# Performance work log

Hardware: AMD Instinct MI355X
Metric: run time of the kernel (lower is better)

The kernel has to match this reference:

```python
import jax, jax.numpy as jnp
import numpy as np

B, S, HID = 2, 2048, 1024
H, HKV, D = 16, 8, 128
G = H // HKV  # GQA group size
EPS = 1e-6
THETA = 1000000.0


def setup_inputs() -> dict:
    key = jax.random.key(0)
    ks = jax.random.split(key, 6)
    hidden_states = jax.random.normal(ks[0], (B, S, HID), dtype=jnp.float32)
    # causal boolean mask: True = attend
    attention_mask = jnp.tril(jnp.ones((S, S), dtype=bool))[None, None]
    # RoPE tables (HF convention: freqs duplicated across both halves)
    inv_freq = 1.0 / (THETA ** (jnp.arange(0, D, 2, dtype=jnp.float32) / D))
    ang = jnp.arange(S, dtype=jnp.float32)[:, None] * inv_freq[None, :]  # [S, D/2]
    emb = jnp.concatenate([ang, ang], axis=-1)  # [S, D]
    cos, sin = jnp.cos(emb), jnp.sin(emb)
    std = 0.02
    Wq = jax.random.normal(ks[1], (HID, H * D), dtype=jnp.float32) * std
    Wk = jax.random.normal(ks[2], (HID, HKV * D), dtype=jnp.float32) * std
    Wv = jax.random.normal(ks[3], (HID, HKV * D), dtype=jnp.float32) * std
    Wo = jax.random.normal(ks[4], (H * D, HID), dtype=jnp.float32) * std
    q_norm_w = jnp.ones((D,), dtype=jnp.float32)
    k_norm_w = jnp.ones((D,), dtype=jnp.float32)
    return {"hidden_states": hidden_states, "attention_mask": attention_mask,
            "cos": cos, "sin": sin, "Wq": Wq, "Wk": Wk, "Wv": Wv, "Wo": Wo,
            "q_norm_w": q_norm_w, "k_norm_w": k_norm_w}


def _rms_norm(x, w):
    var = jnp.mean(x * x, axis=-1, keepdims=True)
    return x * jax.lax.rsqrt(var + EPS) * w


def _rotate_half(x):
    x1, x2 = jnp.split(x, 2, axis=-1)
    return jnp.concatenate([-x2, x1], axis=-1)


def reference(hidden_states, attention_mask, cos, sin, Wq, Wk, Wv, Wo, q_norm_w, k_norm_w):
    b, s, _ = hidden_states.shape
    xq = (hidden_states @ Wq).reshape(b, s, H, D).transpose(0, 2, 1, 3)    # [B,H,S,D]
    xk = (hidden_states @ Wk).reshape(b, s, HKV, D).transpose(0, 2, 1, 3)  # [B,Hkv,S,D]
    xv = (hidden_states @ Wv).reshape(b, s, HKV, D).transpose(0, 2, 1, 3)  # [B,Hkv,S,D]
    xq = _rms_norm(xq, q_norm_w)
    xk = _rms_norm(xk, k_norm_w)
    c = cos[None, None]  # [1,1,S,D]
    si = sin[None, None]
    xq = xq * c + _rotate_half(xq) * si
    xk = xk * c + _rotate_half(xk) * si
    # GQA without materializing repeated KV: group q heads per kv head
    xqg = xq.reshape(b, HKV, G, s, D)
    scale = 1.0 / jnp.sqrt(jnp.asarray(D, dtype=xq.dtype))
    scores = jnp.einsum('bkgsd,bktd->bkgst', xqg, xk) * scale  # [B,Hkv,G,S,S]
    mask = attention_mask[:, :, None]  # [1,1,1,S,S]
    scores = jnp.where(mask, scores, jnp.asarray(-jnp.inf, dtype=scores.dtype))
    probs = jax.nn.softmax(scores, axis=-1)
    out = jnp.einsum('bkgst,bktd->bkgsd', probs, xv)  # [B,Hkv,G,S,D]
    out = out.reshape(b, H, s, D).transpose(0, 2, 1, 3).reshape(b, s, H * D)
    return out @ Wo
```

## Files before the change

kernel.cpp:

```cpp
#include <hip/hip_runtime.h>
#include <stdint.h>

#define B_ 2
#define S_ 2048
#define H_ 16
#define HKV_ 8
#define D_ 128
#define EPS_ 1e-6f
#define SCALE_ 0.08838834764831845f
#define QSZ_ 8388608
#define KSZ_ 4194304

typedef __attribute__((ext_vector_type(8))) __bf16 bf16x8;
typedef __attribute__((ext_vector_type(4))) float f32x4;
typedef __attribute__((ext_vector_type(16))) float f32x16;

static __device__ __forceinline__ uint16_t f2b(float f) {
  uint32_t u = __builtin_bit_cast(uint32_t, f);
  u += 0x7fffu + ((u >> 16) & 1u);
  return (uint16_t)(u >> 16);
}
static __device__ __forceinline__ float b2f(uint16_t b) {
  uint32_t u = ((uint32_t)b) << 16;
  return __builtin_bit_cast(float, u);
}

typedef const __attribute__((address_space(1))) uint32_t* gas_p;
typedef __attribute__((address_space(3))) uint32_t* las_p;
static __device__ __forceinline__ void gload16(const void* g, void* l) {
  __builtin_amdgcn_global_load_lds((gas_p)g, (las_p)l, 16, 0, 0);
}

__global__ void castk(const float* __restrict__ in, uint16_t* __restrict__ out) {
  int i = blockIdx.x * 256 + threadIdx.x;
  float4 f = ((const float4*)in)[i];
  uint2 o;
  o.x = (uint32_t)f2b(f.x) | ((uint32_t)f2b(f.y) << 16);
  o.y = (uint32_t)f2b(f.z) | ((uint32_t)f2b(f.w) << 16);
  ((uint2*)out)[i] = o;
}

__global__ void transcast(const float* __restrict__ Wm, uint16_t* __restrict__ Wt,
                          int K, int N) {
  __shared__ float t[32][33];
  int nb = blockIdx.x * 32, kb = blockIdx.y * 32;
  int tx = threadIdx.x & 31, ty = threadIdx.x >> 5;
  #pragma unroll
  for (int i = ty; i < 32; i += 8) t[i][tx] = Wm[(size_t)(kb + i) * N + nb + tx];
  __syncthreads();
  #pragma unroll
  for (int i = ty; i < 32; i += 8) Wt[(size_t)(nb + i) * K + kb + tx] = f2b(t[tx][i]);
}

__global__ __launch_bounds__(256) void vtrans(const uint16_t* __restrict__ Vin,
                                              uint16_t* __restrict__ Vt) {
  __shared__ uint16_t L[64 * 64];
  int s0 = blockIdx.x * 64, d0 = blockIdx.y * 64;
  const uint16_t* src = Vin + (size_t)blockIdx.z * S_ * D_;
  uint16_t* dst = Vt + (size_t)blockIdx.z * S_ * D_;
  int t = threadIdx.x;
  int rr = t >> 3, cb = t & 7;
  #pragma unroll
  for (int half = 0; half < 2; ++half) {
    int row = rr + half * 32;
    uint4 v = *(const uint4*)(src + (size_t)(s0 + row) * D_ + d0 + cb * 8);
    *(uint4*)(L + row * 64 + ((cb ^ (row & 7)) * 8)) = v;
  }
  __syncthreads();
  int dr = t >> 2, sc = (t & 3) * 16;
  union { uint16_t s[16]; uint4 q[2]; } u;
  #pragma unroll
  for (int j = 0; j < 16; ++j) {
    int s = sc + j;
    u.s[j] = L[s * 64 + (((dr >> 3) ^ (s & 7)) * 8) + (dr & 7)];
  }
  uint4* op = (uint4*)(dst + (size_t)(d0 + dr) * S_ + s0 + sc);
  op[0] = u.q[0];
  op[1] = u.q[1];
}

__global__ __launch_bounds__(256) void gemm_bt(const uint16_t* __restrict__ A,
                                               const uint16_t* __restrict__ Bt,
                                               void* __restrict__ Cout,
                                               int M, int N, int K, int mode) {
  __shared__ uint16_t Al[128 * 64];
  __shared__ uint16_t Bl[128 * 64];
  int tid = threadIdx.x;
  int lane = tid & 63, lr = lane & 15, g = lane >> 4;
  int w = tid >> 6, wm = w >> 1, wn = w & 1;
  int wbase = w * 64;
  int m0 = blockIdx.y * 128, n0 = blockIdx.x * 128;
  f32x4 acc[4][4] = {};
  for (int k0 = 0; k0 < K; k0 += 64) {
    __syncthreads();
    #pragma unroll
    for (int p = 0; p < 4; ++p) {
      int c = tid + p * 256;
      int row = c >> 3, cb = c & 7;
      int sc = (cb ^ (row & 7)) * 8;
      gload16(A + (size_t)(m0 + row) * K + k0 + sc, Al + (size_t)(p * 256 + wbase) * 8);
      gload16(Bt + (size_t)(n0 + row) * K + k0 + sc, Bl + (size_t)(p * 256 + wbase) * 8);
    }
    __syncthreads();
    #pragma unroll
    for (int ks = 0; ks < 2; ++ks) {
      bf16x8 af[4], bfr[4];
      #pragma unroll
      for (int mi = 0; mi < 4; ++mi) {
        int row = wm * 64 + mi * 16 + lr;
        af[mi] = *(bf16x8*)((char*)Al + row * 128 + ((ks * 64 + g * 16) ^ ((row & 7) << 4)));
      }
      #pragma unroll
      for (int ni = 0; ni < 4; ++ni) {
        int row = wn * 64 + ni * 16 + lr;
        bfr[ni] = *(bf16x8*)((char*)Bl + row * 128 + ((ks * 64 + g * 16) ^ ((row & 7) << 4)));
      }
      __builtin_amdgcn_s_setprio(1);
      #pragma unroll
      for (int mi = 0; mi < 4; ++mi)
        #pragma unroll
        for (int ni = 0; ni < 4; ++ni)
          acc[mi][ni] = __builtin_amdgcn_mfma_f32_16x16x32_bf16(af[mi], bfr[ni], acc[mi][ni], 0, 0, 0);
      __builtin_amdgcn_s_setprio(0);
    }
  }
  #pragma unroll
  for (int mi = 0; mi < 4; ++mi)
    #pragma unroll
    for (int ni = 0; ni < 4; ++ni)
      #pragma unroll
      for (int e = 0; e < 4; ++e) {
        int row = m0 + wm * 64 + mi * 16 + 4 * g + e;
        int col = n0 + wn * 64 + ni * 16 + lr;
        float v = acc[mi][ni][e];
        if (mode == 2) {
          ((float*)Cout)[(size_t)row * N + col] = v;
        } else {
          int bb = row >> 11, s = row & 2047;
          size_t off;
          if (col < 2048)
            off = (((size_t)(bb * 16 + (col >> 7))) * 2048 + s) * 128 + (col & 127);
          else if (col < 3072)
            off = QSZ_ + (((size_t)(bb * 8 + ((col - 2048) >> 7))) * 2048 + s) * 128 + (col & 127);
          else
            off = QSZ_ + KSZ_ + (((size_t)(bb * 8 + ((col - 3072) >> 7))) * 2048 + s) * 128 + (col & 127);
          ((uint16_t*)Cout)[off] = f2b(v);
        }
      }
}

__global__ __launch_bounds__(256) void gemm_o(const uint16_t* __restrict__ A,
                                              const uint16_t* __restrict__ Bt,
                                              float* __restrict__ Cout,
                                              int M, int N, int K) {
  __shared__ uint16_t Al[128 * 64];
  __shared__ uint16_t Bl[64 * 64];
  int tid = threadIdx.x;
  int lane = tid & 63, lr = lane & 15, g = lane >> 4;
  int w = tid >> 6, wm = w >> 1, wn = w & 1;
  int wbase = w * 64;
  int m0 = blockIdx.y * 128, n0 = blockIdx.x * 64;
  f32x4 acc[4][2] = {};
  for (int k0 = 0; k0 < K; k0 += 64) {
    __syncthreads();
    #pragma unroll
    for (int p = 0; p < 4; ++p) {
      int c = tid + p * 256;
      int row = c >> 3, cb = c & 7;
      int sc = (cb ^ (row & 7)) * 8;
      gload16(A + (size_t)(m0 + row) * K + k0 + sc, Al + (size_t)(p * 256 + wbase) * 8);
    }
    #pragma unroll
    for (int p = 0; p < 2; ++p) {
      int c = tid + p * 256;
      int row = c >> 3, cb = c & 7;
      int sc = (cb ^ (row & 7)) * 8;
      gload16(Bt + (size_t)(n0 + row) * K + k0 + sc, Bl + (size_t)(p * 256 + wbase) * 8);
    }
    __syncthreads();
    #pragma unroll
    for (int ks = 0; ks < 2; ++ks) {
      bf16x8 af[4], bfr[2];
      #pragma unroll
      for (int mi = 0; mi < 4; ++mi) {
        int row = wm * 64 + mi * 16 + lr;
        af[mi] = *(bf16x8*)((char*)Al + row * 128 + ((ks * 64 + g * 16) ^ ((row & 7) << 4)));
      }
      #pragma unroll
      for (int ni = 0; ni < 2; ++ni) {
        int row = wn * 32 + ni * 16 + lr;
        bfr[ni] = *(bf16x8*)((char*)Bl + row * 128 + ((ks * 64 + g * 16) ^ ((row & 7) << 4)));
      }
      __builtin_amdgcn_s_setprio(1);
      #pragma unroll
      for (int mi = 0; mi < 4; ++mi)
        #pragma unroll
        for (int ni = 0; ni < 2; ++ni)
          acc[mi][ni] = __builtin_amdgcn_mfma_f32_16x16x32_bf16(af[mi], bfr[ni], acc[mi][ni], 0, 0, 0);
      __builtin_amdgcn_s_setprio(0);
    }
  }
  #pragma unroll
  for (int mi = 0; mi < 4; ++mi)
    #pragma unroll
    for (int ni = 0; ni < 2; ++ni)
      #pragma unroll
      for (int e = 0; e < 4; ++e) {
        int row = m0 + wm * 64 + mi * 16 + 4 * g + e;
        int col = n0 + wn * 32 + ni * 16 + lr;
        Cout[(size_t)row * N + col] = acc[mi][ni][e];
      }
}

__global__ void norm_rope(uint16_t* __restrict__ Qb, uint16_t* __restrict__ Kb,
                          const float* __restrict__ qw, const float* __restrict__ kw,
                          const float* __restrict__ cosr, const float* __restrict__ sinr) {
  int row = blockIdx.x * 4 + (threadIdx.x >> 6);
  int lane = threadIdx.x & 63;
  int hh = row % 24;
  int bs = row / 24;
  int b = bs >> 11, s = bs & 2047;
  uint16_t* ptr;
  const float* wv;
  float sc;
  if (hh < H_) { ptr = Qb + (((size_t)(b * H_ + hh)) * S_ + s) * D_; wv = qw; sc = SCALE_; }
  else         { ptr = Kb + (((size_t)(b * HKV_ + (hh - H_))) * S_ + s) * D_; wv = kw; sc = 1.0f; }
  float x1 = b2f(ptr[lane]), x2 = b2f(ptr[lane + 64]);
  float ss = x1 * x1 + x2 * x2;
  #pragma unroll
  for (int msk = 1; msk < 64; msk <<= 1) ss += __shfl_xor(ss, msk, 64);
  float r = rsqrtf(ss * (1.0f / 128.0f) + EPS_);
  float n1 = x1 * r * wv[lane], n2 = x2 * r * wv[lane + 64];
  float c1 = cosr[s * 128 + lane], s1 = sinr[s * 128 + lane];
  float c2 = cosr[s * 128 + lane + 64], s2 = sinr[s * 128 + lane + 64];
  ptr[lane]      = f2b((n1 * c1 - n2 * s1) * sc);
  ptr[lane + 64] = f2b((n2 * c2 + n1 * s2) * sc);
}

#define STAGE(BUF, KB) {                                                       \
  int kb64 = (KB) * 64;                                                        \
  _Pragma("unroll") for (int p2 = 0; p2 < 4; ++p2) {                           \
    int ck = p2 * 4 + w;                                                       \
    int krow = ck * 4 + (lane >> 4);                                           \
    int kg = (lane & 15) ^ (krow & 7);                                         \
    gload16(Kg + (size_t)(kb64 + krow) * D_ + kg * 8, Kl[BUF] + ck * 512);     \
    int vrow = ck * 8 + (lane >> 3);                                           \
    int vg = (lane & 7) ^ (vrow & 7);                                          \
    gload16(Vg + (size_t)vrow * S_ + kb64 + vg * 8, Vl[BUF] + ck * 512);       \
  } }

__global__ __launch_bounds__(256, 2) void attn_kernel(const uint16_t* __restrict__ Qb,
                                                      const uint16_t* __restrict__ Kb,
                                                      const uint16_t* __restrict__ Vtg,
                                                      uint16_t* __restrict__ out) {
  __shared__ uint16_t Kl[2][64 * 128];
  __shared__ uint16_t Vl[2][128 * 64];
  int tid = threadIdx.x, lane = tid & 63, w = tid >> 6;
  int ql = lane & 31, hi = lane >> 5;
  int bi = blockIdx.x;
  int biH = bi >> 8;
  int j = bi & 255;
  int qgl = j >> 5;
  int qg = biH ? qgl : 15 - qgl;
  int rem = j & 31;
  int bkv = rem >> 1, hsel = rem & 1;
  int b = bkv >> 3, kv = bkv & 7, h = kv * 2 + hsel;
  int qt = qg * 4 + w;
  int q0 = qt * 32;
  int mykb = qt >> 1;
  int kbmax = 2 * qg + 1;
  const uint16_t* Qg = Qb + ((size_t)(b * H_ + h)) * S_ * D_;
  const uint16_t* Kg = Kb + ((size_t)(b * HKV_ + kv)) * S_ * D_;
  const uint16_t* Vg = Vtg + ((size_t)(b * HKV_ + kv)) * S_ * D_;
  bf16x8 qf[8];
  #pragma unroll
  for (int t = 0; t < 8; ++t)
    qf[t] = *(const bf16x8*)(Qg + (size_t)(q0 + ql) * D_ + t * 16 + 8 * hi);
  f32x16 O[4] = {};
  float mrun = -__builtin_inff();
  float lrun = 0.f;
  STAGE(0, 0)
  for (int kb = 0; kb <= kbmax; ++kb) {
    int cur = kb & 1;
    __syncthreads();
    if (kb < kbmax) STAGE(cur ^ 1, kb + 1)
    if (kb <= mykb) {
      const uint16_t* KlC = Kl[cur];
      const uint16_t* VlC = Vl[cur];
      bool diag = (kb == mykb);
      bool skip2 = diag && ((qt & 1) == 0);
      float p0[16], p1[16];
      {
        bf16x8 kf[8];
        #pragma unroll
        for (int t = 0; t < 8; ++t)
          kf[t] = *(const bf16x8*)(KlC + ql * 128 + (((2 * t + hi) ^ (ql & 7)) * 8));
        f32x16 acc = {};
        __builtin_amdgcn_s_setprio(1);
        #pragma unroll
        for (int t = 0; t < 8; ++t)
          acc = __builtin_amdgcn_mfma_f32_32x32x16_bf16(kf[t], qf[t], acc, 0, 0, 0);
        __builtin_amdgcn_s_setprio(0);
        #pragma unroll
        for (int r = 0; r < 16; ++r) p0[r] = acc[r];
      }
      if (!skip2) {
        bf16x8 kf[8];
        #pragma unroll
        for (int t = 0; t < 8; ++t)
          kf[t] = *(const bf16x8*)(KlC + (32 + ql) * 128 + (((2 * t + hi) ^ (ql & 7)) * 8));
        f32x16 acc = {};
        __builtin_amdgcn_s_setprio(1);
        #pragma unroll
        for (int t = 0; t < 8; ++t)
          acc = __builtin_amdgcn_mfma_f32_32x32x16_bf16(kf[t], qf[t], acc, 0, 0, 0);
        __builtin_amdgcn_s_setprio(0);
        #pragma unroll
        for (int r = 0; r < 16; ++r) p1[r] = acc[r];
      }
      if (diag && !(qt & 1)) {
        #pragma unroll
        for (int r = 0; r < 16; ++r) {
          int kk = kb * 64 + 8 * (r >> 2) + 4 * hi + (r & 3);
          if (kk > q0 + ql) p0[r] = -__builtin_inff();
        }
      }
      if (diag && (qt & 1)) {
        #pragma unroll
        for (int r = 0; r < 16; ++r) {
          int kk = kb * 64 + 32 + 8 * (r >> 2) + 4 * hi + (r & 3);
          if (kk > q0 + ql) p1[r] = -__builtin_inff();
        }
      }
      float m8[8];
      #pragma unroll
      for (int i = 0; i < 8; ++i) m8[i] = fmaxf(p0[i], p0[i + 8]);
      if (!skip2) {
        #pragma unroll
        for (int i = 0; i < 8; ++i) m8[i] = fmaxf(m8[i], fmaxf(p1[i], p1[i + 8]));
      }
      float m4a = fmaxf(m8[0], m8[4]), m4b = fmaxf(m8[1], m8[5]);
      float m4c = fmaxf(m8[2], m8[6]), m4d = fmaxf(m8[3], m8[7]);
      float pmax = fmaxf(fmaxf(m4a, m4b), fmaxf(m4c, m4d));
      pmax = fmaxf(pmax, __shfl_xor(pmax, 32, 64));
      if (__any(pmax > mrun + 8.f)) {
        float mnew = fmaxf(mrun, pmax);
        float rs = __expf(mrun - mnew);
        lrun *= rs;
        #pragma unroll
        for (int r = 0; r < 16; ++r) {
          float rr = __shfl(rs, (r & 3) + 8 * (r >> 2) + 4 * hi, 64);
          #pragma unroll
          for (int dt = 0; dt < 4; ++dt) O[dt][r] *= rr;
        }
        mrun = mnew;
      }
      float ls = 0.f;
      union PW { uint32_t w[4]; bf16x8 v; } pa0, pa1;
      #pragma unroll
      for (int r = 0; r < 16; ++r) { p0[r] = __expf(p0[r] - mrun); ls += p0[r]; }
      {
        uint32_t uu[4][2];
        #pragma unroll
        for (int T = 0; T < 4; ++T) {
          asm("v_cvt_pk_bf16_f32 %0, %1, %2" : "=v"(uu[T][0]) : "v"(p0[4 * T]), "v"(p0[4 * T + 1]));
          asm("v_cvt_pk_bf16_f32 %0, %1, %2" : "=v"(uu[T][1]) : "v"(p0[4 * T + 2]), "v"(p0[4 * T + 3]));
        }
        uint32_t a = uu[0][0], bb2 = uu[1][0];
        asm("v_permlane32_swap_b32 %0, %1" : "+v"(a), "+v"(bb2));
        uint32_t c = uu[0][1], d = uu[1][1];
        asm("v_permlane32_swap_b32 %0, %1" : "+v"(c), "+v"(d));
        pa0.w[0] = a; pa0.w[1] = c; pa0.w[2] = bb2; pa0.w[3] = d;
        uint32_t a2 = uu[2][0], b2 = uu[3][0];
        asm("v_permlane32_swap_b32 %0, %1" : "+v"(a2), "+v"(b2));
        uint32_t c2 = uu[2][1], d2 = uu[3][1];
        asm("v_permlane32_swap_b32 %0, %1" : "+v"(c2), "+v"(d2));
        pa1.w[0] = a2; pa1.w[1] = c2; pa1.w[2] = b2; pa1.w[3] = d2;
      }
      __builtin_amdgcn_s_setprio(1);
      #pragma unroll
      for (int dt = 0; dt < 4; ++dt) {
        bf16x8 v0 = *(const bf16x8*)(VlC + (dt * 32 + ql) * 64 + (((0 + hi) ^ (ql & 7)) * 8));
        bf16x8 v1 = *(const bf16x8*)(VlC + (dt * 32 + ql) * 64 + (((2 + hi) ^ (ql & 7)) * 8));
        O[dt] = __builtin_amdgcn_mfma_f32_32x32x16_bf16(pa0.v, v0, O[dt], 0, 0, 0);
        O[dt] = __builtin_amdgcn_mfma_f32_32x32x16_bf16(pa1.v, v1, O[dt], 0, 0, 0);
      }
      __builtin_amdgcn_s_setprio(0);
      if (!skip2) {
        union PW pa2, pa3;
        #pragma unroll
        for (int r = 0; r < 16; ++r) { p1[r] = __expf(p1[r] - mrun); ls += p1[r]; }
        {
          uint32_t uu[4][2];
          #pragma unroll
          for (int T = 0; T < 4; ++T) {
            asm("v_cvt_pk_bf16_f32 %0, %1, %2" : "=v"(uu[T][0]) : "v"(p1[4 * T]), "v"(p1[4 * T + 1]));
            asm("v_cvt_pk_bf16_f32 %0, %1, %2" : "=v"(uu[T][1]) : "v"(p1[4 * T + 2]), "v"(p1[4 * T + 3]));
          }
          uint32_t a = uu[0][0], bb2 = uu[1][0];
          asm("v_permlane32_swap_b32 %0, %1" : "+v"(a), "+v"(bb2));
          uint32_t c = uu[0][1], d = uu[1][1];
          asm("v_permlane32_swap_b32 %0, %1" : "+v"(c), "+v"(d));
          pa2.w[0] = a; pa2.w[1] = c; pa2.w[2] = bb2; pa2.w[3] = d;
          uint32_t a2 = uu[2][0], b2 = uu[3][0];
          asm("v_permlane32_swap_b32 %0, %1" : "+v"(a2), "+v"(b2));
          uint32_t c2 = uu[2][1], d2 = uu[3][1];
          asm("v_permlane32_swap_b32 %0, %1" : "+v"(c2), "+v"(d2));
          pa3.w[0] = a2; pa3.w[1] = c2; pa3.w[2] = b2; pa3.w[3] = d2;
        }
        __builtin_amdgcn_s_setprio(1);
        #pragma unroll
        for (int dt = 0; dt < 4; ++dt) {
          bf16x8 v2 = *(const bf16x8*)(VlC + (dt * 32 + ql) * 64 + (((4 + hi) ^ (ql & 7)) * 8));
          bf16x8 v3 = *(const bf16x8*)(VlC + (dt * 32 + ql) * 64 + (((6 + hi) ^ (ql & 7)) * 8));
          O[dt] = __builtin_amdgcn_mfma_f32_32x32x16_bf16(pa2.v, v2, O[dt], 0, 0, 0);
          O[dt] = __builtin_amdgcn_mfma_f32_32x32x16_bf16(pa3.v, v3, O[dt], 0, 0, 0);
        }
        __builtin_amdgcn_s_setprio(0);
      }
      ls += __shfl_xor(ls, 32, 64);
      lrun += ls;
    }
  }
  float linv = 1.0f / lrun;
  #pragma unroll
  for (int r = 0; r < 16; ++r) {
    int qrl = (r & 3) + 8 * (r >> 2) + 4 * hi;
    float lr_ = __shfl(linv, qrl, 64);
    #pragma unroll
    for (int dt = 0; dt < 4; ++dt) {
      size_t o = ((size_t)(b * S_ + q0 + qrl)) * 2048 + h * 128 + dt * 32 + ql;
      out[o] = f2b(O[dt][r] * lr_);
    }
  }
}

extern "C" void kernel_launch(void* const* d_in, const int* in_sizes, int n_in,
                              void* d_out, int out_size, void* d_ws, size_t ws_size,
                              hipStream_t stream) {
  const float* hidden = (const float*)d_in[0];
  const float* cosr = (const float*)d_in[2];
  const float* sinr = (const float*)d_in[3];
  const float* Wq = (const float*)d_in[4];
  const float* Wk = (const float*)d_in[5];
  const float* Wv = (const float*)d_in[6];
  const float* Wo = (const float*)d_in[7];
  const float* qw = (const float*)d_in[8];
  const float* kw = (const float*)d_in[9];

  uint16_t* p = (uint16_t*)d_ws;
  uint16_t* Xb   = p; p += (size_t)4096 * 1024;
  uint16_t* Wqt  = p; p += (size_t)2048 * 1024;
  uint16_t* Wkt  = p; p += (size_t)1024 * 1024;
  uint16_t* Wvt  = p; p += (size_t)1024 * 1024;
  uint16_t* Wot  = p; p += (size_t)1024 * 2048;
  uint16_t* Qbuf = p; p += (size_t)B_ * H_ * S_ * D_;
  uint16_t* Kbuf = p; p += (size_t)B_ * HKV_ * S_ * D_;
  uint16_t* Vbuf = p; p += (size_t)B_ * HKV_ * S_ * D_;
  uint16_t* attn = p; p += (size_t)4096 * 2048;
  uint16_t* Vtb  = Xb;

  castk<<<4096, 256, 0, stream>>>(hidden, Xb);
  transcast<<<dim3(64, 32), 256, 0, stream>>>(Wq, Wqt, 1024, 2048);
  transcast<<<dim3(32, 32), 256, 0, stream>>>(Wk, Wkt, 1024, 1024);
  transcast<<<dim3(32, 32), 256, 0, stream>>>(Wv, Wvt, 1024, 1024);
  transcast<<<dim3(32, 64), 256, 0, stream>>>(Wo, Wot, 2048, 1024);
  gemm_bt<<<dim3(32, 32), 256, 0, stream>>>(Xb, Wqt, Qbuf, 4096, 4096, 1024, 3);
  vtrans<<<dim3(32, 2, 16), 256, 0, stream>>>(Vbuf, Vtb);
  norm_rope<<<24576, 256, 0, stream>>>(Qbuf, Kbuf, qw, kw, cosr, sinr);
  attn_kernel<<<512, 256, 0, stream>>>(Qbuf, Kbuf, Vtb, attn);
  gemm_o<<<dim3(16, 32), 256, 0, stream>>>(attn, Wot, (float*)d_out, 4096, 1024, 2048);
}
```

Baseline: 194.5 us.

## Fuse RMSNorm, RoPE and V transpose into QKV GEMM epilogue; merge prep kernels

The cast and four weight-transpose kernels are merged into one prep launch. The QKV GEMM now stages its output tile in LDS, and its epilogue applies RMSNorm, RoPE and Q scaling for Q/K tiles and writes V already transposed. This removes the separate norm_rope and vtrans kernels, their global round trips and several launches. In exchange the GEMM epilogue uses many registers (64 floats per thread) and issues strided scalar loads of the weight and cos/sin tables.

```diff
diff --git a/kernel.cpp b/kernel.cpp
--- a/kernel.cpp
+++ b/kernel.cpp
@@ -8,8 +8,6 @@
 #define D_ 128
 #define EPS_ 1e-6f
 #define SCALE_ 0.08838834764831845f
-#define QSZ_ 8388608
-#define KSZ_ 4194304
 
 typedef __attribute__((ext_vector_type(8))) __bf16 bf16x8;
 typedef __attribute__((ext_vector_type(4))) float f32x4;
@@ -31,75 +29,69 @@
   __builtin_amdgcn_global_load_lds((gas_p)g, (las_p)l, 16, 0, 0);
 }
 
-__global__ void castk(const float* __restrict__ in, uint16_t* __restrict__ out) {
-  int i = blockIdx.x * 256 + threadIdx.x;
-  float4 f = ((const float4*)in)[i];
-  uint2 o;
-  o.x = (uint32_t)f2b(f.x) | ((uint32_t)f2b(f.y) << 16);
-  o.y = (uint32_t)f2b(f.z) | ((uint32_t)f2b(f.w) << 16);
-  ((uint2*)out)[i] = o;
-}
-
-__global__ void transcast(const float* __restrict__ Wm, uint16_t* __restrict__ Wt,
-                          int K, int N) {
-  __shared__ float t[32][33];
-  int nb = blockIdx.x * 32, kb = blockIdx.y * 32;
+__global__ __launch_bounds__(256) void prep(const float* __restrict__ hidden,
+                                            uint16_t* __restrict__ Xb,
+                                            const float* __restrict__ Wq,
+                                            const float* __restrict__ Wk,
+                                            const float* __restrict__ Wv,
+                                            const float* __restrict__ Wo,
+                                            uint16_t* __restrict__ Wqt,
+                                            uint16_t* __restrict__ Wkt,
+                                            uint16_t* __restrict__ Wvt,
+                                            uint16_t* __restrict__ Wot) {
+  __shared__ float tt[32][33];
+  int bid = blockIdx.x;
+  if (bid < 4096) {
+    int i = bid * 256 + threadIdx.x;
+    float4 f = ((const float4*)hidden)[i];
+    uint2 o;
+    o.x = (uint32_t)f2b(f.x) | ((uint32_t)f2b(f.y) << 16);
+    o.y = (uint32_t)f2b(f.z) | ((uint32_t)f2b(f.w) << 16);
+    ((uint2*)Xb)[i] = o;
+    return;
+  }
+  bid -= 4096;
+  const float* src; uint16_t* dst; int K, N, bx, by;
+  if (bid < 2048)       { src = Wq; dst = Wqt; K = 1024; N = 2048; bx = bid & 63; by = bid >> 6; }
+  else if (bid < 3072)  { bid -= 2048; src = Wk; dst = Wkt; K = 1024; N = 1024; bx = bid & 31; by = bid >> 5; }
+  else if (bid < 4096)  { bid -= 3072; src = Wv; dst = Wvt; K = 1024; N = 1024; bx = bid & 31; by = bid >> 5; }
+  else                  { bid -= 4096; src = Wo; dst = Wot; K = 2048; N = 1024; bx = bid & 31; by = bid >> 5; }
+  int nb = bx * 32, kb = by * 32;
   int tx = threadIdx.x & 31, ty = threadIdx.x >> 5;
   #pragma unroll
-  for (int i = ty; i < 32; i += 8) t[i][tx] = Wm[(size_t)(kb + i) * N + nb + tx];
+  for (int i = ty; i < 32; i += 8) tt[i][tx] = src[(size_t)(kb + i) * N + nb + tx];
   __syncthreads();
   #pragma unroll
-  for (int i = ty; i < 32; i += 8) Wt[(size_t)(nb + i) * K + kb + tx] = f2b(t[tx][i]);
-}
-
-__global__ __launch_bounds__(256) void vtrans(const uint16_t* __restrict__ Vin,
-                                              uint16_t* __restrict__ Vt) {
-  __shared__ uint16_t L[64 * 64];
-  int s0 = blockIdx.x * 64, d0 = blockIdx.y * 64;
-  const uint16_t* src = Vin + (size_t)blockIdx.z * S_ * D_;
-  uint16_t* dst = Vt + (size_t)blockIdx.z * S_ * D_;
-  int t = threadIdx.x;
-  int rr = t >> 3, cb = t & 7;
-  #pragma unroll
-  for (int half = 0; half < 2; ++half) {
-    int row = rr + half * 32;
-    uint4 v = *(const uint4*)(src + (size_t)(s0 + row) * D_ + d0 + cb * 8);
-    *(uint4*)(L + row * 64 + ((cb ^ (row & 7)) * 8)) = v;
-  }
-  __syncthreads();
-  int dr = t >> 2, sc = (t & 3) * 16;
-  union { uint16_t s[16]; uint4 q[2]; } u;
-  #pragma unroll
-  for (int j = 0; j < 16; ++j) {
-    int s = sc + j;
-    u.s[j] = L[s * 64 + (((dr >> 3) ^ (s & 7)) * 8) + (dr & 7)];
-  }
-  uint4* op = (uint4*)(dst + (size_t)(d0 + dr) * S_ + s0 + sc);
-  op[0] = u.q[0];
-  op[1] = u.q[1];
-}
-
-__global__ __launch_bounds__(256) void gemm_bt(const uint16_t* __restrict__ A,
-                                               const uint16_t* __restrict__ Bt,
-                                               void* __restrict__ Cout,
-                                               int M, int N, int K, int mode) {
-  __shared__ uint16_t Al[128 * 64];
-  __shared__ uint16_t Bl[128 * 64];
+  for (int i = ty; i < 32; i += 8) dst[(size_t)(nb + i) * K + kb + tx] = f2b(tt[tx][i]);
+}
+
+__global__ __launch_bounds__(256) void gemm_qkv(const uint16_t* __restrict__ A,
+                                                const uint16_t* __restrict__ Bt,
+                                                uint16_t* __restrict__ Qb,
+                                                uint16_t* __restrict__ Kb,
+                                                uint16_t* __restrict__ Vtb,
+                                                const float* __restrict__ qw,
+                                                const float* __restrict__ kw,
+                                                const float* __restrict__ cosr,
+                                                const float* __restrict__ sinr) {
+  __shared__ uint16_t Sh[128 * 128];
+  uint16_t* Al = Sh;
+  uint16_t* Bl = Sh + 128 * 64;
   int tid = threadIdx.x;
   int lane = tid & 63, lr = lane & 15, g = lane >> 4;
   int w = tid >> 6, wm = w >> 1, wn = w & 1;
   int wbase = w * 64;
   int m0 = blockIdx.y * 128, n0 = blockIdx.x * 128;
   f32x4 acc[4][4] = {};
-  for (int k0 = 0; k0 < K; k0 += 64) {
+  for (int k0 = 0; k0 < 1024; k0 += 64) {
     __syncthreads();
     #pragma unroll
     for (int p = 0; p < 4; ++p) {
       int c = tid + p * 256;
       int row = c >> 3, cb = c & 7;
       int sc = (cb ^ (row & 7)) * 8;
-      gload16(A + (size_t)(m0 + row) * K + k0 + sc, Al + (size_t)(p * 256 + wbase) * 8);
-      gload16(Bt + (size_t)(n0 + row) * K + k0 + sc, Bl + (size_t)(p * 256 + wbase) * 8);
+      gload16(A + (size_t)(m0 + row) * 1024 + k0 + sc, Al + (size_t)(p * 256 + wbase) * 8);
+      gload16(Bt + (size_t)(n0 + row) * 1024 + k0 + sc, Bl + (size_t)(p * 256 + wbase) * 8);
     }
     __syncthreads();
     #pragma unroll
@@ -124,29 +116,75 @@
       __builtin_amdgcn_s_setprio(0);
     }
   }
+  __syncthreads();
+  uint16_t* L = Sh;
   #pragma unroll
   for (int mi = 0; mi < 4; ++mi)
     #pragma unroll
     for (int ni = 0; ni < 4; ++ni)
       #pragma unroll
       for (int e = 0; e < 4; ++e) {
-        int row = m0 + wm * 64 + mi * 16 + 4 * g + e;
-        int col = n0 + wn * 64 + ni * 16 + lr;
-        float v = acc[mi][ni][e];
-        if (mode == 2) {
-          ((float*)Cout)[(size_t)row * N + col] = v;
-        } else {
-          int bb = row >> 11, s = row & 2047;
-          size_t off;
-          if (col < 2048)
-            off = (((size_t)(bb * 16 + (col >> 7))) * 2048 + s) * 128 + (col & 127);
-          else if (col < 3072)
-            off = QSZ_ + (((size_t)(bb * 8 + ((col - 2048) >> 7))) * 2048 + s) * 128 + (col & 127);
-          else
-            off = QSZ_ + KSZ_ + (((size_t)(bb * 8 + ((col - 3072) >> 7))) * 2048 + s) * 128 + (col & 127);
-          ((uint16_t*)Cout)[off] = f2b(v);
-        }
-      }
+        int row = wm * 64 + mi * 16 + 4 * g + e;
+        int col = wn * 64 + ni * 16 + lr;
+        L[row * 128 + ((((col >> 3) ^ (row & 7)) << 3) | (col & 7))] = f2b(acc[mi][ni][e]);
+      }
+  __syncthreads();
+  int hsel = n0 >> 7;
+  if (hsel < 24) {
+    int row = tid >> 1, half = tid & 1;
+    int gr = m0 + row, bb = gr >> 11, s = gr & 2047;
+    int d0 = half * 32;
+    float x[64];
+    #pragma unroll
+    for (int c8 = 0; c8 < 8; ++c8) {
+      int j = (c8 & 3) * 8 + d0 + (c8 >> 2) * 64;
+      union { bf16x8 v; uint16_t u[8]; } tmp;
+      tmp.v = *(bf16x8*)(L + row * 128 + (((j >> 3) ^ (row & 7)) << 3));
+      #pragma unroll
+      for (int k = 0; k < 8; ++k) x[c8 * 8 + k] = b2f(tmp.u[k]);
+    }
+    float ss = 0.f;
+    #pragma unroll
+    for (int k = 0; k < 64; ++k) ss += x[k] * x[k];
+    ss += __shfl_xor(ss, 1, 64);
+    float rn = rsqrtf(ss * (1.0f / 128.0f) + EPS_);
+    const float* wv = (hsel < 16) ? qw : kw;
+    float scq = (hsel < 16) ? SCALE_ : 1.0f;
+    rn *= scq;
+    uint16_t* outp = (hsel < 16)
+      ? Qb + (((size_t)(bb * 16 + hsel)) * 2048 + s) * 128
+      : Kb + (((size_t)(bb * 8 + (hsel - 16))) * 2048 + s) * 128;
+    const float* cR = cosr + s * 128;
+    const float* sR = sinr + s * 128;
+    #pragma unroll
+    for (int c = 0; c < 4; ++c) {
+      int dlo = d0 + c * 8;
+      uint16_t olo[8], ohi[8];
+      #pragma unroll
+      for (int k = 0; k < 8; ++k) {
+        int d = dlo + k;
+        float x1 = x[c * 8 + k] * rn * wv[d];
+        float x2 = x[32 + c * 8 + k] * rn * wv[d + 64];
+        olo[k] = f2b(x1 * cR[d] - x2 * sR[d]);
+        ohi[k] = f2b(x2 * cR[d + 64] + x1 * sR[d + 64]);
+      }
+      *(uint4*)(outp + dlo) = *(uint4*)olo;
+      *(uint4*)(outp + 64 + dlo) = *(uint4*)ohi;
+    }
+  } else {
+    int kvh = hsel - 24;
+    int d0 = tid >> 1, sh = tid & 1;
+    int bb = m0 >> 11, sg0 = (m0 & 2047) + sh * 64;
+    union { uint16_t u[64]; uint4 q[8]; } vv;
+    #pragma unroll
+    for (int sl = 0; sl < 64; ++sl) {
+      int srow = sh * 64 + sl;
+      vv.u[sl] = L[srow * 128 + ((((d0 >> 3) ^ (srow & 7)) << 3) | (d0 & 7))];
+    }
+    uint16_t* vt = Vtb + (((size_t)(bb * 8 + kvh)) * 128 + d0) * 2048 + sg0;
+    #pragma unroll
+    for (int c = 0; c < 8; ++c) *(uint4*)(vt + c * 8) = vv.q[c];
+  }
 }
 
 __global__ __launch_bounds__(256) void gemm_o(const uint16_t* __restrict__ A,
@@ -210,31 +248,6 @@
         int col = n0 + wn * 32 + ni * 16 + lr;
         Cout[(size_t)row * N + col] = acc[mi][ni][e];
       }
-}
-
-__global__ void norm_rope(uint16_t* __restrict__ Qb, uint16_t* __restrict__ Kb,
-                          const float* __restrict__ qw, const float* __restrict__ kw,
-                          const float* __restrict__ cosr, const float* __restrict__ sinr) {
-  int row = blockIdx.x * 4 + (threadIdx.x >> 6);
-  int lane = threadIdx.x & 63;
-  int hh = row % 24;
-  int bs = row / 24;
-  int b = bs >> 11, s = bs & 2047;
-  uint16_t* ptr;
-  const float* wv;
-  float sc;
-  if (hh < H_) { ptr = Qb + (((size_t)(b * H_ + hh)) * S_ + s) * D_; wv = qw; sc = SCALE_; }
-  else         { ptr = Kb + (((size_t)(b * HKV_ + (hh - H_))) * S_ + s) * D_; wv = kw; sc = 1.0f; }
-  float x1 = b2f(ptr[lane]), x2 = b2f(ptr[lane + 64]);
-  float ss = x1 * x1 + x2 * x2;
-  #pragma unroll
-  for (int msk = 1; msk < 64; msk <<= 1) ss += __shfl_xor(ss, msk, 64);
-  float r = rsqrtf(ss * (1.0f / 128.0f) + EPS_);
-  float n1 = x1 * r * wv[lane], n2 = x2 * r * wv[lane + 64];
-  float c1 = cosr[s * 128 + lane], s1 = sinr[s * 128 + lane];
-  float c2 = cosr[s * 128 + lane + 64], s2 = sinr[s * 128 + lane + 64];
-  ptr[lane]      = f2b((n1 * c1 - n2 * s1) * sc);
-  ptr[lane + 64] = f2b((n2 * c2 + n1 * s2) * sc);
 }
 
 #define STAGE(BUF, KB) {                                                       \
@@ -456,18 +469,11 @@
   uint16_t* Wot  = p; p += (size_t)1024 * 2048;
   uint16_t* Qbuf = p; p += (size_t)B_ * H_ * S_ * D_;
   uint16_t* Kbuf = p; p += (size_t)B_ * HKV_ * S_ * D_;
-  uint16_t* Vbuf = p; p += (size_t)B_ * HKV_ * S_ * D_;
+  uint16_t* Vtb  = p; p += (size_t)B_ * HKV_ * S_ * D_;
   uint16_t* attn = p; p += (size_t)4096 * 2048;
-  uint16_t* Vtb  = Xb;
-
-  castk<<<4096, 256, 0, stream>>>(hidden, Xb);
-  transcast<<<dim3(64, 32), 256, 0, stream>>>(Wq, Wqt, 1024, 2048);
-  transcast<<<dim3(32, 32), 256, 0, stream>>>(Wk, Wkt, 1024, 1024);
-  transcast<<<dim3(32, 32), 256, 0, stream>>>(Wv, Wvt, 1024, 1024);
-  transcast<<<dim3(32, 64), 256, 0, stream>>>(Wo, Wot, 2048, 1024);
-  gemm_bt<<<dim3(32, 32), 256, 0, stream>>>(Xb, Wqt, Qbuf, 4096, 4096, 1024, 3);
-  vtrans<<<dim3(32, 2, 16), 256, 0, stream>>>(Vbuf, Vtb);
-  norm_rope<<<24576, 256, 0, stream>>>(Qbuf, Kbuf, qw, kw, cosr, sinr);
+
+  prep<<<10240, 256, 0, stream>>>(hidden, Xb, Wq, Wk, Wv, Wo, Wqt, Wkt, Wvt, Wot);
+  gemm_qkv<<<dim3(32, 32), 256, 0, stream>>>(Xb, Wqt, Qbuf, Kbuf, Vtb, qw, kw, cosr, sinr);
   attn_kernel<<<512, 256, 0, stream>>>(Qbuf, Kbuf, Vtb, attn);
   gemm_o<<<dim3(16, 32), 256, 0, stream>>>(attn, Wot, (float*)d_out, 4096, 1024, 2048);
 }
```

Result: faster. 174.9 us (-10.1%).
